# Optimization experiments

Measured on AMD Instinct MI355X. Metric: run time of the kernel, lower is better.

The kernel has to match this reference:

```python
import jax, jax.numpy as jnp
import numpy as np

N_NODES = 100000   # batch of target nodes
K = 10             # sampled neighbors per node (num_sample default)
VOCAB = 200000     # total graph nodes in embedding table
D = 128            # embed_dim


def setup_inputs() -> dict:
    key = jax.random.key(0)
    k1, k2, k3 = jax.random.split(key, 3)
    embed_table = jax.random.normal(k1, (VOCAB, D), dtype=jnp.float32)
    attn_w = jax.random.normal(k2, (D,), dtype=jnp.float32)
    neigh_idx = jax.random.randint(k3, (N_NODES, K), 0, VOCAB, dtype=jnp.int64)
    return {"embed_table": embed_table, "attn_w": attn_w, "neigh_idx": neigh_idx}


def reference(embed_table, attn_w, neigh_idx):
    # Gather neighbor embeddings: [N, K, D] (the irregular-access hot spot)
    feats = embed_table[neigh_idx]
    # attention_fc: Linear(D, 1, bias=False) -> scores [N, K]
    scores = jnp.einsum("nkd,d->nk", feats, attn_w)
    # softmax over the neighbor axis (dim=0 in the per-node torch loop == K here)
    weights = jax.nn.softmax(scores, axis=1)
    # attention-weighted sum of neighbor features -> [N, D]
    out = jnp.einsum("nk,nkd->nd", weights, feats)
    return out
```

## Files before the change

kernel.cpp:

```cpp
#include <hip/hip_runtime.h>
#include <math.h>


#define KNEIGH  10
#define DIM     128
#define QMAX    126.5f
#define WSTRIDE 12

__global__ __launch_bounds__(256) void convert_q8_kernel(
    const float*  __restrict__ table,
    const float*  __restrict__ attn_w,
    unsigned int* __restrict__ q8,
    float2*       __restrict__ aux,
    int vocab)
{
    const int gtid = blockIdx.x * blockDim.x + threadIdx.x;
    const int lane = threadIdx.x & 63;
    const int half = lane >> 5;
    const int sub  = lane & 31;
    const int row  = (gtid >> 6) * 2 + half;
    if (row >= vocab) return;

    const float4 f  = *(const float4*)(table + (size_t)row * DIM + sub * 4);
    const float4 w4 = *(const float4*)(attn_w + sub * 4);

    float p = f.x * w4.x + f.y * w4.y + f.z * w4.z + f.w * w4.w;
    float am = fmaxf(fmaxf(fabsf(f.x), fabsf(f.y)),
                     fmaxf(fabsf(f.z), fabsf(f.w)));
    #pragma unroll
    for (int off = 16; off >= 1; off >>= 1) {
        p  += __shfl_xor(p, off, 64);
        am  = fmaxf(am, __shfl_xor(am, off, 64));
    }

    const float scale = am * (1.0f / QMAX);
    const float inv   = (am > 0.f) ? (QMAX / am) : 0.f;

    const int q0 = (int)rintf(f.x * inv) + 128;
    const int q1 = (int)rintf(f.y * inv) + 128;
    const int q2 = (int)rintf(f.z * inv) + 128;
    const int q3 = (int)rintf(f.w * inv) + 128;
    q8[(size_t)row * 32 + sub] =
        (unsigned)q0 | ((unsigned)q1 << 8) | ((unsigned)q2 << 16) |
        ((unsigned)q3 << 24);

    if (sub == 0) aux[row] = make_float2(p, scale);
}

__global__ __launch_bounds__(256) void weights_kernel(
    const float2* __restrict__ aux,
    const int*    __restrict__ idx,
    float*        __restrict__ wt,
    int n_nodes)
{
    const int node = blockIdx.x * blockDim.x + threadIdx.x;
    if (node >= n_nodes) return;

    const int2* ip = (const int2*)(idx + (size_t)node * KNEIGH);
    const int2 i01 = ip[0], i23 = ip[1], i45 = ip[2], i67 = ip[3], i89 = ip[4];

    const float2 a0 = aux[i01.x], a1 = aux[i01.y], a2 = aux[i23.x],
                 a3 = aux[i23.y], a4 = aux[i45.x], a5 = aux[i45.y],
                 a6 = aux[i67.x], a7 = aux[i67.y], a8 = aux[i89.x],
                 a9 = aux[i89.y];

    const float m = fmaxf(fmaxf(fmaxf(fmaxf(a0.x, a1.x), fmaxf(a2.x, a3.x)),
                                fmaxf(fmaxf(a4.x, a5.x), fmaxf(a6.x, a7.x))),
                          fmaxf(a8.x, a9.x));
    const float e0 = __expf(a0.x - m), e1 = __expf(a1.x - m),
                e2 = __expf(a2.x - m), e3 = __expf(a3.x - m),
                e4 = __expf(a4.x - m), e5 = __expf(a5.x - m),
                e6 = __expf(a6.x - m), e7 = __expf(a7.x - m),
                e8 = __expf(a8.x - m), e9 = __expf(a9.x - m);
    const float inv = 1.0f / (e0 + e1 + e2 + e3 + e4 + e5 + e6 + e7 + e8 + e9);

    const float t0 = e0 * inv * a0.y, t1 = e1 * inv * a1.y,
                t2 = e2 * inv * a2.y, t3 = e3 * inv * a3.y,
                t4 = e4 * inv * a4.y, t5 = e5 * inv * a5.y,
                t6 = e6 * inv * a6.y, t7 = e7 * inv * a7.y,
                t8 = e8 * inv * a8.y, t9 = e9 * inv * a9.y;
    const float C = -128.f * (t0 + t1 + t2 + t3 + t4 + t5 + t6 + t7 + t8 + t9);

    float4* wp = (float4*)(wt + (size_t)node * WSTRIDE);
    wp[0] = make_float4(t0, t1, t2, t3);
    wp[1] = make_float4(t4, t5, t6, t7);
    wp[2] = make_float4(t8, t9, C, 0.f);
}

__global__ __launch_bounds__(256, 8) void attn_gather_q8_kernel(
    const unsigned int* __restrict__ q8,
    const float*        __restrict__ wt,
    const int*          __restrict__ idx,
    float*              __restrict__ out,
    int n_nodes)
{
    const int gtid = blockIdx.x * blockDim.x + threadIdx.x;
    const int wid  = gtid >> 6;
    const int n0   = __builtin_amdgcn_readfirstlane(wid * 2);
    if (n0 >= n_nodes) return;
    const int  n1   = n0 + 1;
    const bool has1 = (n1 < n_nodes);
    const int  lane = threadIdx.x & 63;
    const int  q    = lane >> 4;
    const int  sub  = lane & 15;

    const int b0 = n0 * KNEIGH;
    const int b1 = has1 ? b0 + KNEIGH : b0;

    const int ia0 = idx[b0+0], ia1 = idx[b0+1], ia2 = idx[b0+2], ia3 = idx[b0+3],
              ia4 = idx[b0+4], ia5 = idx[b0+5], ia6 = idx[b0+6], ia7 = idx[b0+7],
              ia8 = idx[b0+8], ia9 = idx[b0+9];
    const int ib0 = idx[b1+0], ib1 = idx[b1+1], ib2 = idx[b1+2], ib3 = idx[b1+3],
              ib4 = idx[b1+4], ib5 = idx[b1+5], ib6 = idx[b1+6], ib7 = idx[b1+7],
              ib8 = idx[b1+8], ib9 = idx[b1+9];

    const int r0 = (q == 0) ? ia0 : (q == 1) ? ia1 : (q == 2) ? ia2 : ia3;
    const int r1 = (q == 0) ? ia4 : (q == 1) ? ia5 : (q == 2) ? ia6 : ia7;
    const int r2 = (q == 0) ? ia8 : (q == 1) ? ia9 : (q == 2) ? ib0 : ib1;
    const int r3 = (q == 0) ? ib2 : (q == 1) ? ib3 : (q == 2) ? ib4 : ib5;
    const int r4 = (q == 0) ? ib6 : (q == 1) ? ib7 : (q == 2) ? ib8 : ib9;

    const uint2 g0 = *(const uint2*)(q8 + (size_t)r0 * 32 + sub * 2);
    const uint2 g1 = *(const uint2*)(q8 + (size_t)r1 * 32 + sub * 2);
    const uint2 g2 = *(const uint2*)(q8 + (size_t)r2 * 32 + sub * 2);
    const uint2 g3 = *(const uint2*)(q8 + (size_t)r3 * 32 + sub * 2);
    const uint2 g4 = *(const uint2*)(q8 + (size_t)r4 * 32 + sub * 2);

    const float* wa = wt + (size_t)n0 * WSTRIDE;
    const float* wb = wt + (size_t)(has1 ? n1 : n0) * WSTRIDE;
    const float ta0 = wa[0], ta1 = wa[1], ta2 = wa[2], ta3 = wa[3],
                ta4 = wa[4], ta5 = wa[5], ta6 = wa[6], ta7 = wa[7],
                ta8 = wa[8], ta9 = wa[9], Ca = wa[10];
    const float tb0 = wb[0], tb1 = wb[1], tb2 = wb[2], tb3 = wb[3],
                tb4 = wb[4], tb5 = wb[5], tb6 = wb[6], tb7 = wb[7],
                tb8 = wb[8], tb9 = wb[9], Cb = wb[10];

    const float w0 = (q == 0) ? ta0 : (q == 1) ? ta1 : (q == 2) ? ta2 : ta3;
    const float w1 = (q == 0) ? ta4 : (q == 1) ? ta5 : (q == 2) ? ta6 : ta7;
    const float w2 = (q == 0) ? ta8 : (q == 1) ? ta9 : (q == 2) ? tb0 : tb1;
    const float w3 = (q == 0) ? tb2 : (q == 1) ? tb3 : (q == 2) ? tb4 : tb5;
    const float w4 = (q == 0) ? tb6 : (q == 1) ? tb7 : (q == 2) ? tb8 : tb9;

    float a0=0.f,a1=0.f,a2=0.f,a3=0.f,a4=0.f,a5=0.f,a6=0.f,a7=0.f;
    float b0f=0.f,b1f=0.f,b2f=0.f,b3f=0.f,b4f=0.f,b5f=0.f,b6f=0.f,b7f=0.f;

    #define UNPK(G, W, A0,A1,A2,A3,A4,A5,A6,A7)                                \
        A0 = fmaf((W), (float)((G).x & 0xffu),         A0);                    \
        A1 = fmaf((W), (float)(((G).x >> 8) & 0xffu),  A1);                    \
        A2 = fmaf((W), (float)(((G).x >> 16) & 0xffu), A2);                    \
        A3 = fmaf((W), (float)((G).x >> 24),           A3);                    \
        A4 = fmaf((W), (float)((G).y & 0xffu),         A4);                    \
        A5 = fmaf((W), (float)(((G).y >> 8) & 0xffu),  A5);                    \
        A6 = fmaf((W), (float)(((G).y >> 16) & 0xffu), A6);                    \
        A7 = fmaf((W), (float)((G).y >> 24),           A7);

    UNPK(g0, w0, a0,a1,a2,a3,a4,a5,a6,a7)
    UNPK(g1, w1, a0,a1,a2,a3,a4,a5,a6,a7)
    {
        float c0=0.f,c1=0.f,c2=0.f,c3=0.f,c4=0.f,c5=0.f,c6=0.f,c7=0.f;
        UNPK(g2, w2, c0,c1,c2,c3,c4,c5,c6,c7)
        const bool lo = (q < 2);
        a0 += lo ? c0 : 0.f; a1 += lo ? c1 : 0.f; a2 += lo ? c2 : 0.f;
        a3 += lo ? c3 : 0.f; a4 += lo ? c4 : 0.f; a5 += lo ? c5 : 0.f;
        a6 += lo ? c6 : 0.f; a7 += lo ? c7 : 0.f;
        b0f += lo ? 0.f : c0; b1f += lo ? 0.f : c1; b2f += lo ? 0.f : c2;
        b3f += lo ? 0.f : c3; b4f += lo ? 0.f : c4; b5f += lo ? 0.f : c5;
        b6f += lo ? 0.f : c6; b7f += lo ? 0.f : c7;
    }
    UNPK(g3, w3, b0f,b1f,b2f,b3f,b4f,b5f,b6f,b7f)
    UNPK(g4, w4, b0f,b1f,b2f,b3f,b4f,b5f,b6f,b7f)
    #undef UNPK

    #define RED(X) X += __shfl_xor(X, 16, 64); X += __shfl_xor(X, 32, 64);
    RED(a0) RED(a1) RED(a2) RED(a3) RED(a4) RED(a5) RED(a6) RED(a7)
    RED(b0f) RED(b1f) RED(b2f) RED(b3f) RED(b4f) RED(b5f) RED(b6f) RED(b7f)
    #undef RED

    if (q == 0) {
        float* p = out + (size_t)n0 * DIM + sub * 8;
        *(float4*)(p)     = make_float4(a0 + Ca, a1 + Ca, a2 + Ca, a3 + Ca);
        *(float4*)(p + 4) = make_float4(a4 + Ca, a5 + Ca, a6 + Ca, a7 + Ca);
    } else if (q == 1 && has1) {
        float* p = out + (size_t)n1 * DIM + sub * 8;
        *(float4*)(p)     = make_float4(b0f + Cb, b1f + Cb, b2f + Cb, b3f + Cb);
        *(float4*)(p + 4) = make_float4(b4f + Cb, b5f + Cb, b6f + Cb, b7f + Cb);
    }
}

__global__ __launch_bounds__(256) void attn_agg_fp32_kernel(
    const float* __restrict__ table,
    const float* __restrict__ attn_w,
    const int*   __restrict__ idx,
    float*       __restrict__ out,
    int n_nodes)
{
    const int gtid = blockIdx.x * blockDim.x + threadIdx.x;
    const int node = gtid >> 6;
    const int lane = threadIdx.x & 63;
    if (node >= n_nodes) return;

    const float2 wv = *(const float2*)(attn_w + lane * 2);
    int my_idx = 0;
    if (lane < KNEIGH) my_idx = idx[node * KNEIGH + lane];

    float2 f[KNEIGH];
    float  s[KNEIGH];
    #pragma unroll
    for (int k = 0; k < KNEIGH; ++k) {
        const int id = __shfl(my_idx, k, 64);
        f[k] = *(const float2*)(table + (size_t)id * DIM + lane * 2);
        float p = f[k].x * wv.x + f[k].y * wv.y;
        #pragma unroll
        for (int off = 32; off >= 1; off >>= 1)
            p += __shfl_xor(p, off, 64);
        s[k] = p;
    }
    float m = s[0];
    #pragma unroll
    for (int k = 1; k < KNEIGH; ++k) m = fmaxf(m, s[k]);
    float denom = 0.f;
    #pragma unroll
    for (int k = 0; k < KNEIGH; ++k) { s[k] = __expf(s[k] - m); denom += s[k]; }
    const float inv = 1.0f / denom;
    float2 acc = make_float2(0.f, 0.f);
    #pragma unroll
    for (int k = 0; k < KNEIGH; ++k) {
        const float wk = s[k] * inv;
        acc.x = fmaf(wk, f[k].x, acc.x);
        acc.y = fmaf(wk, f[k].y, acc.y);
    }
    *(float2*)(out + (size_t)node * DIM + lane * 2) = acc;
}

extern "C" void kernel_launch(void* const* d_in, const int* in_sizes, int n_in,
                              void* d_out, int out_size, void* d_ws, size_t ws_size,
                              hipStream_t stream) {
    const float* table  = (const float*)d_in[0];
    const float* attn_w = (const float*)d_in[1];
    const int*   idx    = (const int*)d_in[2];
    float*       out    = (float*)d_out;

    const int vocab   = in_sizes[0] / DIM;
    const int n_nodes = in_sizes[2] / KNEIGH;

    const size_t q8_bytes  = (size_t)vocab * DIM;
    const size_t aux_bytes = (size_t)vocab * sizeof(float2);
    const size_t wt_bytes  = (size_t)n_nodes * WSTRIDE * sizeof(float);
    const size_t need      = q8_bytes + aux_bytes + wt_bytes;

    if (ws_size >= need) {
        unsigned int* q8  = (unsigned int*)d_ws;
        float2*       aux = (float2*)((char*)d_ws + q8_bytes);
        float*        wt  = (float*)((char*)d_ws + q8_bytes + aux_bytes);

        const int waves1  = (vocab + 1) / 2;
        const int blocks1 = (waves1 + 3) / 4;
        convert_q8_kernel<<<blocks1, 256, 0, stream>>>(
            table, attn_w, q8, aux, vocab);

        const int blocksW = (n_nodes + 255) / 256;
        weights_kernel<<<blocksW, 256, 0, stream>>>(
            aux, idx, wt, n_nodes);

        const int waves2  = (n_nodes + 1) / 2;
        const int blocks2 = (waves2 + 3) / 4;
        attn_gather_q8_kernel<<<blocks2, 256, 0, stream>>>(
            q8, wt, idx, out, n_nodes);
    } else {
        const int blocks = (n_nodes + 3) / 4;
        attn_agg_fp32_kernel<<<blocks, 256, 0, stream>>>(
            table, attn_w, idx, out, n_nodes);
    }
}
```

Before: 194.7 us.

## Map four nodes per wave with one node per quarter-wave in q8 gather

The gather kernel now gives each 16-lane quarter of a wave a whole node, so a wave handles four nodes instead of two. Each lane issues ten 8-byte gathers and reads its node's weights as three float4 loads. This removes the cross-quarter shuffle reduction and the select logic that split node contributions. The cost is more loads in flight and more registers per lane, so the occupancy hint drops from 8 to 6, and each wave reads four nodes' index rows through scalar-like loads.

```diff
diff --git a/kernel.cpp b/kernel.cpp
--- a/kernel.cpp
+++ b/kernel.cpp
@@ -87,7 +87,7 @@
     wp[2] = make_float4(t8, t9, C, 0.f);
 }
 
-__global__ __launch_bounds__(256, 8) void attn_gather_q8_kernel(
+__global__ __launch_bounds__(256, 6) void attn_gather_q8_kernel(
     const unsigned int* __restrict__ q8,
     const float*        __restrict__ wt,
     const int*          __restrict__ idx,
@@ -96,94 +96,83 @@
 {
     const int gtid = blockIdx.x * blockDim.x + threadIdx.x;
     const int wid  = gtid >> 6;
-    const int n0   = __builtin_amdgcn_readfirstlane(wid * 2);
-    if (n0 >= n_nodes) return;
-    const int  n1   = n0 + 1;
-    const bool has1 = (n1 < n_nodes);
-    const int  lane = threadIdx.x & 63;
-    const int  q    = lane >> 4;
-    const int  sub  = lane & 15;
-
-    const int b0 = n0 * KNEIGH;
-    const int b1 = has1 ? b0 + KNEIGH : b0;
-
-    const int ia0 = idx[b0+0], ia1 = idx[b0+1], ia2 = idx[b0+2], ia3 = idx[b0+3],
-              ia4 = idx[b0+4], ia5 = idx[b0+5], ia6 = idx[b0+6], ia7 = idx[b0+7],
-              ia8 = idx[b0+8], ia9 = idx[b0+9];
-    const int ib0 = idx[b1+0], ib1 = idx[b1+1], ib2 = idx[b1+2], ib3 = idx[b1+3],
-              ib4 = idx[b1+4], ib5 = idx[b1+5], ib6 = idx[b1+6], ib7 = idx[b1+7],
-              ib8 = idx[b1+8], ib9 = idx[b1+9];
-
-    const int r0 = (q == 0) ? ia0 : (q == 1) ? ia1 : (q == 2) ? ia2 : ia3;
-    const int r1 = (q == 0) ? ia4 : (q == 1) ? ia5 : (q == 2) ? ia6 : ia7;
-    const int r2 = (q == 0) ? ia8 : (q == 1) ? ia9 : (q == 2) ? ib0 : ib1;
-    const int r3 = (q == 0) ? ib2 : (q == 1) ? ib3 : (q == 2) ? ib4 : ib5;
-    const int r4 = (q == 0) ? ib6 : (q == 1) ? ib7 : (q == 2) ? ib8 : ib9;
+    const int nb   = __builtin_amdgcn_readfirstlane(wid * 4);
+    if (nb >= n_nodes) return;
+    const int lane = threadIdx.x & 63;
+    const int q    = lane >> 4;
+    const int sub  = lane & 15;
+
+    const int lim = n_nodes - 1;
+    const int na = nb;
+    const int n1 = (nb + 1 < n_nodes) ? nb + 1 : lim;
+    const int n2 = (nb + 2 < n_nodes) ? nb + 2 : lim;
+    const int n3 = (nb + 3 < n_nodes) ? nb + 3 : lim;
+    const int ba = na * KNEIGH, bb = n1 * KNEIGH,
+              bc = n2 * KNEIGH, bd = n3 * KNEIGH;
+
+    const int ia0 = idx[ba+0], ia1 = idx[ba+1], ia2 = idx[ba+2], ia3 = idx[ba+3],
+              ia4 = idx[ba+4], ia5 = idx[ba+5], ia6 = idx[ba+6], ia7 = idx[ba+7],
+              ia8 = idx[ba+8], ia9 = idx[ba+9];
+    const int ib0 = idx[bb+0], ib1 = idx[bb+1], ib2 = idx[bb+2], ib3 = idx[bb+3],
+              ib4 = idx[bb+4], ib5 = idx[bb+5], ib6 = idx[bb+6], ib7 = idx[bb+7],
+              ib8 = idx[bb+8], ib9 = idx[bb+9];
+    const int ic0 = idx[bc+0], ic1 = idx[bc+1], ic2 = idx[bc+2], ic3 = idx[bc+3],
+              ic4 = idx[bc+4], ic5 = idx[bc+5], ic6 = idx[bc+6], ic7 = idx[bc+7],
+              ic8 = idx[bc+8], ic9 = idx[bc+9];
+    const int id0 = idx[bd+0], id1 = idx[bd+1], id2 = idx[bd+2], id3 = idx[bd+3],
+              id4 = idx[bd+4], id5 = idx[bd+5], id6 = idx[bd+6], id7 = idx[bd+7],
+              id8 = idx[bd+8], id9 = idx[bd+9];
+
+    #define SEL4(A,B,C,D) ((q == 0) ? (A) : (q == 1) ? (B) : (q == 2) ? (C) : (D))
+    const int r0 = SEL4(ia0, ib0, ic0, id0);
+    const int r1 = SEL4(ia1, ib1, ic1, id1);
+    const int r2 = SEL4(ia2, ib2, ic2, id2);
+    const int r3 = SEL4(ia3, ib3, ic3, id3);
+    const int r4 = SEL4(ia4, ib4, ic4, id4);
+    const int r5 = SEL4(ia5, ib5, ic5, id5);
+    const int r6 = SEL4(ia6, ib6, ic6, id6);
+    const int r7 = SEL4(ia7, ib7, ic7, id7);
+    const int r8 = SEL4(ia8, ib8, ic8, id8);
+    const int r9 = SEL4(ia9, ib9, ic9, id9);
+    #undef SEL4
 
     const uint2 g0 = *(const uint2*)(q8 + (size_t)r0 * 32 + sub * 2);
     const uint2 g1 = *(const uint2*)(q8 + (size_t)r1 * 32 + sub * 2);
     const uint2 g2 = *(const uint2*)(q8 + (size_t)r2 * 32 + sub * 2);
     const uint2 g3 = *(const uint2*)(q8 + (size_t)r3 * 32 + sub * 2);
     const uint2 g4 = *(const uint2*)(q8 + (size_t)r4 * 32 + sub * 2);
-
-    const float* wa = wt + (size_t)n0 * WSTRIDE;
-    const float* wb = wt + (size_t)(has1 ? n1 : n0) * WSTRIDE;
-    const float ta0 = wa[0], ta1 = wa[1], ta2 = wa[2], ta3 = wa[3],
-                ta4 = wa[4], ta5 = wa[5], ta6 = wa[6], ta7 = wa[7],
-                ta8 = wa[8], ta9 = wa[9], Ca = wa[10];
-    const float tb0 = wb[0], tb1 = wb[1], tb2 = wb[2], tb3 = wb[3],
-                tb4 = wb[4], tb5 = wb[5], tb6 = wb[6], tb7 = wb[7],
-                tb8 = wb[8], tb9 = wb[9], Cb = wb[10];
-
-    const float w0 = (q == 0) ? ta0 : (q == 1) ? ta1 : (q == 2) ? ta2 : ta3;
-    const float w1 = (q == 0) ? ta4 : (q == 1) ? ta5 : (q == 2) ? ta6 : ta7;
-    const float w2 = (q == 0) ? ta8 : (q == 1) ? ta9 : (q == 2) ? tb0 : tb1;
-    const float w3 = (q == 0) ? tb2 : (q == 1) ? tb3 : (q == 2) ? tb4 : tb5;
-    const float w4 = (q == 0) ? tb6 : (q == 1) ? tb7 : (q == 2) ? tb8 : tb9;
+    const uint2 g5 = *(const uint2*)(q8 + (size_t)r5 * 32 + sub * 2);
+    const uint2 g6 = *(const uint2*)(q8 + (size_t)r6 * 32 + sub * 2);
+    const uint2 g7 = *(const uint2*)(q8 + (size_t)r7 * 32 + sub * 2);
+    const uint2 g8 = *(const uint2*)(q8 + (size_t)r8 * 32 + sub * 2);
+    const uint2 g9 = *(const uint2*)(q8 + (size_t)r9 * 32 + sub * 2);
+
+    const int myn = (nb + q < n_nodes) ? nb + q : lim;
+    const float4* wp = (const float4*)(wt + (size_t)myn * WSTRIDE);
+    const float4 w03 = wp[0];
+    const float4 w47 = wp[1];
+    const float4 w8C = wp[2];
 
     float a0=0.f,a1=0.f,a2=0.f,a3=0.f,a4=0.f,a5=0.f,a6=0.f,a7=0.f;
-    float b0f=0.f,b1f=0.f,b2f=0.f,b3f=0.f,b4f=0.f,b5f=0.f,b6f=0.f,b7f=0.f;
-
-    #define UNPK(G, W, A0,A1,A2,A3,A4,A5,A6,A7)                                \
-        A0 = fmaf((W), (float)((G).x & 0xffu),         A0);                    \
-        A1 = fmaf((W), (float)(((G).x >> 8) & 0xffu),  A1);                    \
-        A2 = fmaf((W), (float)(((G).x >> 16) & 0xffu), A2);                    \
-        A3 = fmaf((W), (float)((G).x >> 24),           A3);                    \
-        A4 = fmaf((W), (float)((G).y & 0xffu),         A4);                    \
-        A5 = fmaf((W), (float)(((G).y >> 8) & 0xffu),  A5);                    \
-        A6 = fmaf((W), (float)(((G).y >> 16) & 0xffu), A6);                    \
-        A7 = fmaf((W), (float)((G).y >> 24),           A7);
-
-    UNPK(g0, w0, a0,a1,a2,a3,a4,a5,a6,a7)
-    UNPK(g1, w1, a0,a1,a2,a3,a4,a5,a6,a7)
-    {
-        float c0=0.f,c1=0.f,c2=0.f,c3=0.f,c4=0.f,c5=0.f,c6=0.f,c7=0.f;
-        UNPK(g2, w2, c0,c1,c2,c3,c4,c5,c6,c7)
-        const bool lo = (q < 2);
-        a0 += lo ? c0 : 0.f; a1 += lo ? c1 : 0.f; a2 += lo ? c2 : 0.f;
-        a3 += lo ? c3 : 0.f; a4 += lo ? c4 : 0.f; a5 += lo ? c5 : 0.f;
-        a6 += lo ? c6 : 0.f; a7 += lo ? c7 : 0.f;
-        b0f += lo ? 0.f : c0; b1f += lo ? 0.f : c1; b2f += lo ? 0.f : c2;
-        b3f += lo ? 0.f : c3; b4f += lo ? 0.f : c4; b5f += lo ? 0.f : c5;
-        b6f += lo ? 0.f : c6; b7f += lo ? 0.f : c7;
-    }
-    UNPK(g3, w3, b0f,b1f,b2f,b3f,b4f,b5f,b6f,b7f)
-    UNPK(g4, w4, b0f,b1f,b2f,b3f,b4f,b5f,b6f,b7f)
+    #define UNPK(G, W)                                                         \
+        a0 = fmaf((W), (float)((G).x & 0xffu),         a0);                    \
+        a1 = fmaf((W), (float)(((G).x >> 8) & 0xffu),  a1);                    \
+        a2 = fmaf((W), (float)(((G).x >> 16) & 0xffu), a2);                    \
+        a3 = fmaf((W), (float)((G).x >> 24),           a3);                    \
+        a4 = fmaf((W), (float)((G).y & 0xffu),         a4);                    \
+        a5 = fmaf((W), (float)(((G).y >> 8) & 0xffu),  a5);                    \
+        a6 = fmaf((W), (float)(((G).y >> 16) & 0xffu), a6);                    \
+        a7 = fmaf((W), (float)((G).y >> 24),           a7);
+    UNPK(g0, w03.x) UNPK(g1, w03.y) UNPK(g2, w03.z) UNPK(g3, w03.w)
+    UNPK(g4, w47.x) UNPK(g5, w47.y) UNPK(g6, w47.z) UNPK(g7, w47.w)
+    UNPK(g8, w8C.x) UNPK(g9, w8C.y)
     #undef UNPK
 
-    #define RED(X) X += __shfl_xor(X, 16, 64); X += __shfl_xor(X, 32, 64);
-    RED(a0) RED(a1) RED(a2) RED(a3) RED(a4) RED(a5) RED(a6) RED(a7)
-    RED(b0f) RED(b1f) RED(b2f) RED(b3f) RED(b4f) RED(b5f) RED(b6f) RED(b7f)
-    #undef RED
-
-    if (q == 0) {
-        float* p = out + (size_t)n0 * DIM + sub * 8;
-        *(float4*)(p)     = make_float4(a0 + Ca, a1 + Ca, a2 + Ca, a3 + Ca);
-        *(float4*)(p + 4) = make_float4(a4 + Ca, a5 + Ca, a6 + Ca, a7 + Ca);
-    } else if (q == 1 && has1) {
-        float* p = out + (size_t)n1 * DIM + sub * 8;
-        *(float4*)(p)     = make_float4(b0f + Cb, b1f + Cb, b2f + Cb, b3f + Cb);
-        *(float4*)(p + 4) = make_float4(b4f + Cb, b5f + Cb, b6f + Cb, b7f + Cb);
+    const float C = w8C.z;
+    if (nb + q < n_nodes) {
+        float* p = out + (size_t)(nb + q) * DIM + sub * 8;
+        *(float4*)(p)     = make_float4(a0 + C, a1 + C, a2 + C, a3 + C);
+        *(float4*)(p + 4) = make_float4(a4 + C, a5 + C, a6 + C, a7 + C);
     }
 }
 
@@ -262,7 +251,7 @@
         weights_kernel<<<blocksW, 256, 0, stream>>>(
             aux, idx, wt, n_nodes);
 
-        const int waves2  = (n_nodes + 1) / 2;
+        const int waves2  = (n_nodes + 3) / 4;
         const int blocks2 = (waves2 + 3) / 4;
         attn_gather_q8_kernel<<<blocks2, 256, 0, stream>>>(
             q8, wt, idx, out, n_nodes);
```

Result: no change. 192.7 us (-1.0%).
